# Optimization experiments

Hardware: AMD Instinct MI355X
Metric: run time of the kernel (lower is better)

The kernel has to match this reference:

```python
import jax, jax.numpy as jnp
import numpy as np

N_HEAD = 16
NEG = -1.0e9


def setup_inputs() -> dict:
    key = jax.random.key(0)
    k1, k2, k3 = jax.random.split(key, 3)
    B, T, C = 4, 2048, 1024
    x = jax.random.normal(k1, (B, T, C), dtype=jnp.float32)
    # torch Linear(C, 3C, bias=False): weight [3C, C], y = x @ W.T
    w_attn = jax.random.normal(k2, (3 * C, C), dtype=jnp.float32) * (1.0 / np.sqrt(C))
    w_proj = jax.random.normal(k3, (C, C), dtype=jnp.float32) * (1.0 / np.sqrt(C))
    return {"x": x, "w_attn": w_attn, "w_proj": w_proj}


def reference(x, w_attn, w_proj):
    B, T, C = x.shape
    hd = C // N_HEAD
    qkv = x @ w_attn.T  # [B,T,3C]
    q, k, v = jnp.split(qkv, 3, axis=2)
    # [B,T,C] -> [B,H,T,hd]
    q = q.reshape(B, T, N_HEAD, hd).transpose(0, 2, 1, 3)
    k = k.reshape(B, T, N_HEAD, hd).transpose(0, 2, 1, 3)
    v = v.reshape(B, T, N_HEAD, hd).transpose(0, 2, 1, 3)
    att = jnp.einsum('bhqd,bhkd->bhqk', q, k) * (1.0 / np.sqrt(hd))
    causal = jnp.tril(jnp.ones((T, T), dtype=bool))
    att = jnp.where(causal[None, None, :, :], att, NEG)
    att = jax.nn.softmax(att, axis=-1)
    y = jnp.einsum('bhqk,bhkd->bhqd', att, v)  # [B,H,T,hd]
    y = y.transpose(0, 2, 1, 3).reshape(B, T, C)
    return y @ w_proj.T
```

## Files before the change

kernel.cpp:

```cpp
#include <hip/hip_runtime.h>
#include <hip/hip_bf16.h>

typedef __bf16 bf16x8_t __attribute__((ext_vector_type(8)));
typedef __bf16 bf16x4_t __attribute__((ext_vector_type(4)));
typedef float f32x4_t __attribute__((ext_vector_type(4)));

__device__ __forceinline__ void gload_lds16(const void* g, void* l) {
    __builtin_amdgcn_global_load_lds((const __attribute__((address_space(1))) void*)g,
                                     (__attribute__((address_space(3))) void*)l, 16, 0, 0);
}

__global__ void f2bf_kernel(const float* __restrict__ in, __bf16* __restrict__ out, int n) {
    int i = (blockIdx.x * blockDim.x + threadIdx.x) * 4;
    if (i >= n) return;
    float4 v = *(const float4*)(in + i);
    bf16x4_t o;
    o[0] = (__bf16)v.x; o[1] = (__bf16)v.y; o[2] = (__bf16)v.z; o[3] = (__bf16)v.w;
    *(bf16x4_t*)(out + i) = o;
}

__global__ __launch_bounds__(512, 2) void gemm1_8ph(const __bf16* __restrict__ A,
                                                    const __bf16* __restrict__ Bt,
                                                    __bf16* __restrict__ C,
                                                    int M, int N, int K) {
    __shared__ __bf16 AsB[2][16 * 512];
    __shared__ __bf16 BsB[2][32 * 512];

    const int tid  = threadIdx.x;
    const int lane = tid & 63;
    const int wid  = tid >> 6;
    const int wm   = wid >> 2;
    const int wn   = wid & 3;

    const int nwg   = gridDim.x;
    const int ntile = N >> 8;
    int fl = blockIdx.x;
    fl = (fl & 7) * (nwg >> 3) + (fl >> 3);
    const int m0 = (fl / ntile) * 128;
    const int n0 = (fl % ntile) * 256;

    const int lr = lane & 15;
    const int lg = lane >> 4;
    const int cr = lg * 4;
    const int srow = lane >> 3;
    const int gcol = (((lane & 7) ^ srow) << 3);

    f32x4_t acc[4][4];
#pragma unroll
    for (int i = 0; i < 4; ++i)
#pragma unroll
        for (int j = 0; j < 4; ++j)
            acc[i][j] = (f32x4_t){0.f, 0.f, 0.f, 0.f};

    const int NT = K >> 6;

    auto stage = [&](int kt, int buf) {
        const __bf16* Ab = A + (size_t)m0 * K + kt * 64;
        const __bf16* Bb = Bt + (size_t)n0 * K + kt * 64;
        __bf16* Al = &AsB[buf][0];
        __bf16* Bl = &BsB[buf][0];
#pragma unroll
        for (int j = 0; j < 6; ++j) {
            int seg = wid * 6 + j;
            if (seg < 16) {
                gload_lds16(Ab + (size_t)(seg * 8 + srow) * K + gcol, Al + seg * 512);
            } else {
                int s2 = seg - 16;
                gload_lds16(Bb + (size_t)(s2 * 8 + srow) * K + gcol, Bl + s2 * 512);
            }
        }
    };

    stage(0, 0);

    for (int kt = 0; kt < NT; ++kt) {
        const int cur = kt & 1;
        const bool pf = (kt + 1 < NT);
        if (pf) stage(kt + 1, cur ^ 1);

        if (pf) asm volatile("s_waitcnt vmcnt(6)" ::: "memory");
        else    asm volatile("s_waitcnt vmcnt(0)" ::: "memory");
        __builtin_amdgcn_sched_barrier(0);
        __builtin_amdgcn_s_barrier();
        __builtin_amdgcn_sched_barrier(0);

        const __bf16* Al = &AsB[cur][0];
        const __bf16* Bl = &BsB[cur][0];

        bf16x8_t af[4][2];
#pragma unroll
        for (int mf = 0; mf < 4; ++mf)
#pragma unroll
            for (int kk = 0; kk < 2; ++kk) {
                const int row = wm * 64 + mf * 16 + lr;
                const int g   = kk * 4 + lg;
                af[mf][kk] = *(const bf16x8_t*)&Al[row * 64 + ((g ^ (row & 7)) << 3)];
            }

#pragma unroll
        for (int p = 0; p < 2; ++p) {
            bf16x8_t bfr[2][2];
#pragma unroll
            for (int nfp = 0; nfp < 2; ++nfp)
#pragma unroll
                for (int kk = 0; kk < 2; ++kk) {
                    const int row = wn * 64 + (p * 2 + nfp) * 16 + lr;
                    const int g   = kk * 4 + lg;
                    bfr[nfp][kk] = *(const bf16x8_t*)&Bl[row * 64 + ((g ^ (row & 7)) << 3)];
                }
            __builtin_amdgcn_s_setprio(1);
#pragma unroll
            for (int mf = 0; mf < 4; ++mf)
#pragma unroll
                for (int nfp = 0; nfp < 2; ++nfp) {
                    const int nf = p * 2 + nfp;
                    acc[mf][nf] = __builtin_amdgcn_mfma_f32_16x16x32_bf16(af[mf][0], bfr[nfp][0], acc[mf][nf], 0, 0, 0);
                    acc[mf][nf] = __builtin_amdgcn_mfma_f32_16x16x32_bf16(af[mf][1], bfr[nfp][1], acc[mf][nf], 0, 0, 0);
                }
            __builtin_amdgcn_s_setprio(0);
            __builtin_amdgcn_s_barrier();
        }
        __builtin_amdgcn_sched_barrier(0);
    }

#pragma unroll
    for (int mf = 0; mf < 4; ++mf)
#pragma unroll
        for (int nf = 0; nf < 4; ++nf)
#pragma unroll
            for (int r = 0; r < 4; ++r) {
                int row = m0 + wm * 64 + mf * 16 + cr + r;
                int col = n0 + wn * 64 + nf * 16 + lr;
                C[(size_t)row * N + col] = (__bf16)acc[mf][nf][r];
            }
}

template <typename OutT>
__global__ __launch_bounds__(256) void gemm_bt(const __bf16* __restrict__ A,
                                               const __bf16* __restrict__ Bt,
                                               OutT* __restrict__ C,
                                               int M, int N, int K) {
    __shared__ __bf16 As[128 * 32];
    __shared__ __bf16 Bs[128 * 32];

    const int tid  = threadIdx.x;
    const int lane = tid & 63;
    const int wid  = tid >> 6;
    const int wm   = wid >> 1;
    const int wn   = wid & 1;

    const int nwg = gridDim.x * gridDim.y;
    int fl = blockIdx.y * gridDim.x + blockIdx.x;
    fl = (fl & 7) * (nwg >> 3) + (fl >> 3);
    const int m0 = (fl / gridDim.x) * 128;
    const int n0 = (fl % gridDim.x) * 128;

    const int lr = lane & 15;
    const int lk = (lane >> 4) * 8;
    const int cr = (lane >> 4) * 4;

    f32x4_t acc[4][4];
    for (int i = 0; i < 4; ++i)
        for (int j = 0; j < 4; ++j)
            acc[i][j] = (f32x4_t){0.f, 0.f, 0.f, 0.f};

    for (int k0 = 0; k0 < K; k0 += 32) {
        __syncthreads();
        for (int i = 0; i < 2; ++i) {
            int flat = i * 256 + tid;
            int row  = flat >> 2;
            int col  = (flat & 3) * 8;
            gload_lds16(&A[(size_t)(m0 + row) * K + k0 + col], &As[(size_t)(i * 256 + wid * 64) * 8]);
            gload_lds16(&Bt[(size_t)(n0 + row) * K + k0 + col], &Bs[(size_t)(i * 256 + wid * 64) * 8]);
        }
        __syncthreads();

        bf16x8_t af[4], bfr[4];
        for (int mf = 0; mf < 4; ++mf)
            af[mf] = *(const bf16x8_t*)&As[(wm * 64 + mf * 16 + lr) * 32 + lk];
        for (int nf = 0; nf < 4; ++nf)
            bfr[nf] = *(const bf16x8_t*)&Bs[(wn * 64 + nf * 16 + lr) * 32 + lk];
        for (int mf = 0; mf < 4; ++mf)
            for (int nf = 0; nf < 4; ++nf)
                acc[mf][nf] = __builtin_amdgcn_mfma_f32_16x16x32_bf16(af[mf], bfr[nf], acc[mf][nf], 0, 0, 0);
    }

    for (int mf = 0; mf < 4; ++mf)
        for (int nf = 0; nf < 4; ++nf)
            for (int r = 0; r < 4; ++r) {
                int row = m0 + wm * 64 + mf * 16 + cr + r;
                int col = n0 + wn * 64 + nf * 16 + lr;
                C[(size_t)row * N + col] = (OutT)acc[mf][nf][r];
            }
}

__global__ __launch_bounds__(512, 4) void attn_kernel(const __bf16* __restrict__ qkv,
                                                      __bf16* __restrict__ y) {
    const int T = 2048, C3 = 3072;
    const int orig = blockIdx.x;
    const int bidx = ((orig & 7) << 6) + (orig >> 3);
    const int pair = bidx & 7;
    const int h    = (bidx >> 3) & 15;
    const int b    = bidx >> 7;

    __shared__ __bf16 Ks[128 * 64];
    __shared__ __bf16 Vt[2][64 * 72];
    __shared__ __bf16 Ps[8 * 16 * 136];

    const int tid  = threadIdx.x;
    const int lane = tid & 63;
    const int w    = tid >> 6;
    const int lr   = lane & 15;
    const int lg   = lane >> 4;
    const int lk   = lg * 8;

    const __bf16* qg = qkv + (size_t)b * T * C3 + h * 64;
    const __bf16* kg = qg + 1024;
    const __bf16* vg = qg + 2048;

    const float CE    = 0.125f * 1.44269504f;
    const float DEFER = 44.0f;

    const int r0    = tid >> 3;
    const int kcol  = (tid & 7) * 8;
    const int kslot = ((tid & 7) ^ (r0 & 7)) << 3;
    const int vks   = r0 ^ ((tid & 7) << 3);

    __bf16* Pw = &Ps[w * 16 * 136];

    for (int pass = 0; pass < 2; ++pass) {
        const int qs  = pass ? 15 - pair : pair;
        const int qt0 = qs * 128;
        const int nt  = qs + 1;

        bf16x8_t qf0, qf1;
        {
            const __bf16* qrow = qg + (size_t)(qt0 + w * 16 + lr) * C3;
            qf0 = *(const bf16x8_t*)&qrow[lk];
            qf1 = *(const bf16x8_t*)&qrow[32 + lk];
        }

        bf16x8_t ka = *(const bf16x8_t*)&kg[(size_t)r0 * C3 + kcol];
        bf16x8_t kb = *(const bf16x8_t*)&kg[(size_t)(64 + r0) * C3 + kcol];
        bf16x8_t va = *(const bf16x8_t*)&vg[(size_t)r0 * C3 + kcol];
        bf16x8_t vb = *(const bf16x8_t*)&vg[(size_t)(64 + r0) * C3 + kcol];

        f32x4_t o_acc[4];
#pragma unroll
        for (int i = 0; i < 4; ++i) o_acc[i] = (f32x4_t){0.f, 0.f, 0.f, 0.f};
        float m_r = -3.0e38f, l_r = 0.f;

        for (int t = 0; t < nt; ++t) {
            __syncthreads();

            *(bf16x8_t*)&Ks[r0 * 64 + kslot] = ka;
            *(bf16x8_t*)&Ks[(64 + r0) * 64 + kslot] = kb;
#pragma unroll
            for (int j = 0; j < 8; ++j) Vt[0][(kcol + j) * 72 + vks] = va[j];
#pragma unroll
            for (int j = 0; j < 8; ++j) Vt[1][(kcol + j) * 72 + vks] = vb[j];

            __syncthreads();

            if (t + 1 < nt) {
                const size_t kb0 = (size_t)(t + 1) * 128;
                ka = *(const bf16x8_t*)&kg[(kb0 + r0) * C3 + kcol];
                kb = *(const bf16x8_t*)&kg[(kb0 + 64 + r0) * C3 + kcol];
                va = *(const bf16x8_t*)&vg[(kb0 + r0) * C3 + kcol];
                vb = *(const bf16x8_t*)&vg[(kb0 + 64 + r0) * C3 + kcol];
            }

            f32x4_t s[8];
#pragma unroll
            for (int c = 0; c < 8; ++c) {
                const int key = c * 16 + lr;
                const int sw  = (key & 7) << 3;
                bf16x8_t kfa = *(const bf16x8_t*)&Ks[key * 64 + (lk ^ sw)];
                bf16x8_t kfb = *(const bf16x8_t*)&Ks[key * 64 + ((32 + lk) ^ sw)];
                s[c] = __builtin_amdgcn_mfma_f32_16x16x32_bf16(kfa, qf0, (f32x4_t){0.f, 0.f, 0.f, 0.f}, 0, 0, 0);
                s[c] = __builtin_amdgcn_mfma_f32_16x16x32_bf16(kfb, qf1, s[c], 0, 0, 0);
            }

            if (t == nt - 1) {
                const int ql = w * 16 + lr;
#pragma unroll
                for (int c = 0; c < 8; ++c)
#pragma unroll
                    for (int r = 0; r < 4; ++r)
                        if (c * 16 + lg * 4 + r > ql) s[c][r] = -1.0e30f;
            }

            float pm = s[0][0];
#pragma unroll
            for (int c = 0; c < 8; ++c)
#pragma unroll
                for (int r = 0; r < 4; ++r) pm = fmaxf(pm, s[c][r]);

            if (!__all(pm <= m_r + DEFER)) {
                pm = fmaxf(pm, __shfl_xor(pm, 16));
                pm = fmaxf(pm, __shfl_xor(pm, 32));
                const float mn    = fmaxf(m_r, pm);
                const float alpha = exp2f((m_r - mn) * CE);
                l_r *= alpha;
#pragma unroll
                for (int dt = 0; dt < 4; ++dt)
#pragma unroll
                    for (int r = 0; r < 4; ++r) o_acc[dt][r] *= alpha;
                m_r = mn;
            }
            const float mce = m_r * CE;

            float rs = 0.f;
#pragma unroll
            for (int c = 0; c < 8; ++c) {
                bf16x4_t pk;
#pragma unroll
                for (int r = 0; r < 4; ++r) {
                    float pv = exp2f(fmaf(s[c][r], CE, -mce));
                    rs += pv;
                    pk[r] = (__bf16)pv;
                }
                *(bf16x4_t*)&Pw[lr * 136 + c * 16 + lg * 4] = pk;
            }
            rs += __shfl_xor(rs, 16);
            rs += __shfl_xor(rs, 32);
            l_r += rs;

#pragma unroll
            for (int hf = 0; hf < 2; ++hf) {
                bf16x8_t pb0 = *(const bf16x8_t*)&Pw[lr * 136 + hf * 64 + lk];
                bf16x8_t pb1 = *(const bf16x8_t*)&Pw[lr * 136 + hf * 64 + 32 + lk];
#pragma unroll
                for (int dt = 0; dt < 4; ++dt) {
                    const int d   = dt * 16 + lr;
                    const int sw2 = ((d >> 3) & 7) << 3;
                    bf16x8_t vb0 = *(const bf16x8_t*)&Vt[hf][d * 72 + (lk ^ sw2)];
                    bf16x8_t vb1 = *(const bf16x8_t*)&Vt[hf][d * 72 + ((32 + lk) ^ sw2)];
                    o_acc[dt] = __builtin_amdgcn_mfma_f32_16x16x32_bf16(vb0, pb0, o_acc[dt], 0, 0, 0);
                    o_acc[dt] = __builtin_amdgcn_mfma_f32_16x16x32_bf16(vb1, pb1, o_acc[dt], 0, 0, 0);
                }
            }
        }

        const float inv = 1.0f / l_r;
        const int q = qt0 + w * 16 + lr;
#pragma unroll
        for (int dt = 0; dt < 4; ++dt) {
            bf16x4_t ov;
#pragma unroll
            for (int r = 0; r < 4; ++r) ov[r] = (__bf16)(o_acc[dt][r] * inv);
            *(bf16x4_t*)&y[(size_t)(b * T + q) * 1024 + h * 64 + dt * 16 + lg * 4] = ov;
        }
    }
}

extern "C" void kernel_launch(void* const* d_in, const int* in_sizes, int n_in,
                              void* d_out, int out_size, void* d_ws, size_t ws_size,
                              hipStream_t stream) {
    const float* x      = (const float*)d_in[0];
    const float* w_attn = (const float*)d_in[1];
    const float* w_proj = (const float*)d_in[2];
    float* out = (float*)d_out;

    char* ws = (char*)d_ws;
    __bf16* xb   = (__bf16*)(ws);
    __bf16* wab  = (__bf16*)(ws + 16777216);
    __bf16* wpb  = (__bf16*)(ws + 23068672);
    __bf16* qkvb = (__bf16*)(ws + 25165824);
    __bf16* yb   = (__bf16*)(ws + 75497472);

    f2bf_kernel<<<8192, 256, 0, stream>>>(x, xb, 8388608);
    f2bf_kernel<<<3072, 256, 0, stream>>>(w_attn, wab, 3145728);
    f2bf_kernel<<<1024, 256, 0, stream>>>(w_proj, wpb, 1048576);

    gemm1_8ph<<<768, 512, 0, stream>>>(xb, wab, qkvb, 8192, 3072, 1024);

    attn_kernel<<<512, 512, 0, stream>>>(qkvb, yb);

    gemm_bt<float><<<dim3(8, 64), 256, 0, stream>>>(yb, wpb, out, 8192, 1024, 1024);
}
```

Baseline: 188.6 us.

## Write V pre-transposed from QKV GEMM epilogue to avoid LDS transpose in attention

The QKV GEMM epilogue now writes Q and K into a 2048-wide buffer and V into a separate per-head transposed [b,h,d,t] layout. The attention kernel then loads V rows with vectorized 16-byte LDS stores using an XOR swizzle, replacing the scalar element-by-element transpose into LDS. This removes many scalar LDS writes and bank conflicts in the attention inner loop. The cost is strided 8-byte global stores for V in the GEMM epilogue, which may hurt its write coalescing.

```diff
diff --git a/kernel.cpp b/kernel.cpp
--- a/kernel.cpp
+++ b/kernel.cpp
@@ -21,7 +21,8 @@
 
 __global__ __launch_bounds__(512, 2) void gemm1_8ph(const __bf16* __restrict__ A,
                                                     const __bf16* __restrict__ Bt,
-                                                    __bf16* __restrict__ C,
+                                                    __bf16* __restrict__ Cqk,
+                                                    __bf16* __restrict__ Vg,
                                                     int M, int N, int K) {
     __shared__ __bf16 AsB[2][16 * 512];
     __shared__ __bf16 BsB[2][32 * 512];
@@ -123,16 +124,34 @@
         __builtin_amdgcn_sched_barrier(0);
     }
 
-#pragma unroll
-    for (int mf = 0; mf < 4; ++mf)
-#pragma unroll
-        for (int nf = 0; nf < 4; ++nf)
-#pragma unroll
-            for (int r = 0; r < 4; ++r) {
-                int row = m0 + wm * 64 + mf * 16 + cr + r;
-                int col = n0 + wn * 64 + nf * 16 + lr;
-                C[(size_t)row * N + col] = (__bf16)acc[mf][nf][r];
-            }
+    if (n0 < 2048) {
+#pragma unroll
+        for (int mf = 0; mf < 4; ++mf)
+#pragma unroll
+            for (int nf = 0; nf < 4; ++nf)
+#pragma unroll
+                for (int r = 0; r < 4; ++r) {
+                    int row = m0 + wm * 64 + mf * 16 + cr + r;
+                    int col = n0 + wn * 64 + nf * 16 + lr;
+                    Cqk[(size_t)row * 2048 + col] = (__bf16)acc[mf][nf][r];
+                }
+    } else {
+#pragma unroll
+        for (int mf = 0; mf < 4; ++mf) {
+            const int row0 = m0 + wm * 64 + mf * 16 + cr;
+            const int bb   = row0 >> 11;
+            const int tt   = row0 & 2047;
+#pragma unroll
+            for (int nf = 0; nf < 4; ++nf) {
+                const int c3 = n0 + wn * 64 + nf * 16 + lr - 2048;
+                const int hh = c3 >> 6, dd = c3 & 63;
+                bf16x4_t pv;
+#pragma unroll
+                for (int r = 0; r < 4; ++r) pv[r] = (__bf16)acc[mf][nf][r];
+                *(bf16x4_t*)&Vg[((size_t)(bb * 16 + hh) * 64 + dd) * 2048 + tt] = pv;
+            }
+        }
+    }
 }
 
 template <typename OutT>
@@ -195,8 +214,9 @@
 }
 
 __global__ __launch_bounds__(512, 4) void attn_kernel(const __bf16* __restrict__ qkv,
+                                                      const __bf16* __restrict__ Vg,
                                                       __bf16* __restrict__ y) {
-    const int T = 2048, C3 = 3072;
+    const int T = 2048, LD = 2048;
     const int orig = blockIdx.x;
     const int bidx = ((orig & 7) << 6) + (orig >> 3);
     const int pair = bidx & 7;
@@ -204,7 +224,7 @@
     const int b    = bidx >> 7;
 
     __shared__ __bf16 Ks[128 * 64];
-    __shared__ __bf16 Vt[2][64 * 72];
+    __shared__ __bf16 Vt[64 * 128];
     __shared__ __bf16 Ps[8 * 16 * 136];
 
     const int tid  = threadIdx.x;
@@ -214,9 +234,9 @@
     const int lg   = lane >> 4;
     const int lk   = lg * 8;
 
-    const __bf16* qg = qkv + (size_t)b * T * C3 + h * 64;
-    const __bf16* kg = qg + 1024;
-    const __bf16* vg = qg + 2048;
+    const __bf16* qg  = qkv + (size_t)b * T * LD + h * 64;
+    const __bf16* kg  = qg + 1024;
+    const __bf16* Vgb = Vg + (size_t)(b * 16 + h) * 64 * 2048;
 
     const float CE    = 0.125f * 1.44269504f;
     const float DEFER = 44.0f;
@@ -224,7 +244,8 @@
     const int r0    = tid >> 3;
     const int kcol  = (tid & 7) * 8;
     const int kslot = ((tid & 7) ^ (r0 & 7)) << 3;
-    const int vks   = r0 ^ ((tid & 7) << 3);
+    const int vd  = tid >> 3;
+    const int vc0 = tid & 7;
 
     __bf16* Pw = &Ps[w * 16 * 136];
 
@@ -235,15 +256,15 @@
 
         bf16x8_t qf0, qf1;
         {
-            const __bf16* qrow = qg + (size_t)(qt0 + w * 16 + lr) * C3;
+            const __bf16* qrow = qg + (size_t)(qt0 + w * 16 + lr) * LD;
             qf0 = *(const bf16x8_t*)&qrow[lk];
             qf1 = *(const bf16x8_t*)&qrow[32 + lk];
         }
 
-        bf16x8_t ka = *(const bf16x8_t*)&kg[(size_t)r0 * C3 + kcol];
-        bf16x8_t kb = *(const bf16x8_t*)&kg[(size_t)(64 + r0) * C3 + kcol];
-        bf16x8_t va = *(const bf16x8_t*)&vg[(size_t)r0 * C3 + kcol];
-        bf16x8_t vb = *(const bf16x8_t*)&vg[(size_t)(64 + r0) * C3 + kcol];
+        bf16x8_t ka = *(const bf16x8_t*)&kg[(size_t)r0 * LD + kcol];
+        bf16x8_t kb = *(const bf16x8_t*)&kg[(size_t)(64 + r0) * LD + kcol];
+        bf16x8_t va = *(const bf16x8_t*)&Vgb[(size_t)vd * 2048 + vc0 * 8];
+        bf16x8_t vb = *(const bf16x8_t*)&Vgb[(size_t)vd * 2048 + (vc0 + 8) * 8];
 
         f32x4_t o_acc[4];
 #pragma unroll
@@ -255,19 +276,17 @@
 
             *(bf16x8_t*)&Ks[r0 * 64 + kslot] = ka;
             *(bf16x8_t*)&Ks[(64 + r0) * 64 + kslot] = kb;
-#pragma unroll
-            for (int j = 0; j < 8; ++j) Vt[0][(kcol + j) * 72 + vks] = va[j];
-#pragma unroll
-            for (int j = 0; j < 8; ++j) Vt[1][(kcol + j) * 72 + vks] = vb[j];
+            *(bf16x8_t*)&Vt[vd * 128 + ((vc0 ^ (vd & 7)) << 3)] = va;
+            *(bf16x8_t*)&Vt[vd * 128 + (((vc0 + 8) ^ (vd & 7)) << 3)] = vb;
 
             __syncthreads();
 
             if (t + 1 < nt) {
                 const size_t kb0 = (size_t)(t + 1) * 128;
-                ka = *(const bf16x8_t*)&kg[(kb0 + r0) * C3 + kcol];
-                kb = *(const bf16x8_t*)&kg[(kb0 + 64 + r0) * C3 + kcol];
-                va = *(const bf16x8_t*)&vg[(kb0 + r0) * C3 + kcol];
-                vb = *(const bf16x8_t*)&vg[(kb0 + 64 + r0) * C3 + kcol];
+                ka = *(const bf16x8_t*)&kg[(kb0 + r0) * LD + kcol];
+                kb = *(const bf16x8_t*)&kg[(kb0 + 64 + r0) * LD + kcol];
+                va = *(const bf16x8_t*)&Vgb[(size_t)vd * 2048 + kb0 + vc0 * 8];
+                vb = *(const bf16x8_t*)&Vgb[(size_t)vd * 2048 + kb0 + (vc0 + 8) * 8];
             }
 
             f32x4_t s[8];
@@ -332,10 +351,9 @@
                 bf16x8_t pb1 = *(const bf16x8_t*)&Pw[lr * 136 + hf * 64 + 32 + lk];
 #pragma unroll
                 for (int dt = 0; dt < 4; ++dt) {
-                    const int d   = dt * 16 + lr;
-                    const int sw2 = ((d >> 3) & 7) << 3;
-                    bf16x8_t vb0 = *(const bf16x8_t*)&Vt[hf][d * 72 + (lk ^ sw2)];
-                    bf16x8_t vb1 = *(const bf16x8_t*)&Vt[hf][d * 72 + ((32 + lk) ^ sw2)];
+                    const int d = dt * 16 + lr;
+                    bf16x8_t vb0 = *(const bf16x8_t*)&Vt[d * 128 + (((hf * 8 + lg) ^ (d & 7)) << 3)];
+                    bf16x8_t vb1 = *(const bf16x8_t*)&Vt[d * 128 + (((hf * 8 + 4 + lg) ^ (d & 7)) << 3)];
                     o_acc[dt] = __builtin_amdgcn_mfma_f32_16x16x32_bf16(vb0, pb0, o_acc[dt], 0, 0, 0);
                     o_acc[dt] = __builtin_amdgcn_mfma_f32_16x16x32_bf16(vb1, pb1, o_acc[dt], 0, 0, 0);
                 }
@@ -367,15 +385,16 @@
     __bf16* wab  = (__bf16*)(ws + 16777216);
     __bf16* wpb  = (__bf16*)(ws + 23068672);
     __bf16* qkvb = (__bf16*)(ws + 25165824);
-    __bf16* yb   = (__bf16*)(ws + 75497472);
+    __bf16* yb   = (__bf16*)(ws + 58720256);
+    __bf16* Vg   = (__bf16*)(ws + 75497472);
 
     f2bf_kernel<<<8192, 256, 0, stream>>>(x, xb, 8388608);
     f2bf_kernel<<<3072, 256, 0, stream>>>(w_attn, wab, 3145728);
     f2bf_kernel<<<1024, 256, 0, stream>>>(w_proj, wpb, 1048576);
 
-    gemm1_8ph<<<768, 512, 0, stream>>>(xb, wab, qkvb, 8192, 3072, 1024);
-
-    attn_kernel<<<512, 512, 0, stream>>>(qkvb, yb);
+    gemm1_8ph<<<768, 512, 0, stream>>>(xb, wab, qkvb, Vg, 8192, 3072, 1024);
+
+    attn_kernel<<<512, 512, 0, stream>>>(qkvb, Vg, yb);
 
     gemm_bt<float><<<dim3(8, 64), 256, 0, stream>>>(yb, wpb, out, 8192, 1024, 1024);
 }
```

Result: no change. 188.2 us (-0.2%).
